# Kernel tuning notes

Measured on AMD Instinct MI355X. Metric: run time of the kernel, lower is better.

## Reference

```python
import jax, jax.numpy as jnp
import numpy as np

GROUPS = 8   # channels // group_size with group_size=8 for C=64
EPS = 1e-5


def group_norm_qc(x0, x1, gamma, beta):
    """LatticeGroupNorm: stats computed jointly over both cosets per (batch, group)."""
    B, C, H, W = x0.shape
    g = GROUPS
    xg = jnp.concatenate([x0.reshape(B, g, -1), x1.reshape(B, g, -1)], axis=-1)
    mean = xg.mean(axis=-1).reshape(B, g, 1, 1, 1)
    var = xg.var(axis=-1).reshape(B, g, 1, 1, 1)
    inv = jax.lax.rsqrt(var + EPS)
    ga = gamma[None, :, None, None]
    be = beta[None, :, None, None]

    def norm(x):
        xr = x.reshape(B, g, C // g, H, W)
        return ((xr - mean) * inv).reshape(B, C, H, W) * ga + be

    return norm(x0), norm(x1)


def qc_conv(x0, x1, w_center, w_corner, bias):
    """Quincunx LatticePad+LatticeConvolution with stencil
    [(0,0),(2,0),(0,2),(2,2),(1,1)], center (1,1).
    w_center: [O,I] tap (1,1) (same-coset 1x1).
    w_corner: [O,I,2,2] taps (0,0),(2,0),(0,2),(2,2) (cross-coset 2x2).
    Pad keeps output cosets the same size as inputs ('same' lattice conv)."""
    dn = ('NCHW', 'OIHW', 'NCHW')

    def c1(x):
        return jnp.einsum('oi,bihw->bohw', w_center, x)

    def c2(x, pad):
        return jax.lax.conv_general_dilated(x, w_corner, (1, 1), pad,
                                            dimension_numbers=dn)

    b = bias[None, :, None, None]
    # coset0 output gathers coset1 at (i-1+a, j-1+b) -> pad top/left
    out0 = c1(x0) + c2(x1, ((1, 0), (1, 0))) + b
    # coset1 output gathers coset0 at (i+a, j+b) -> pad bottom/right
    out1 = c1(x1) + c2(x0, ((0, 1), (0, 1))) + b
    return out0, out1


def setup_inputs() -> dict:
    key = jax.random.key(0)
    ks = jax.random.split(key, 10)
    B, C, H, W = 2, 64, 256, 256
    s = 0.05
    return {
        'x0': jax.random.normal(ks[0], (B, C, H, W), jnp.float32),
        'x1': jax.random.normal(ks[1], (B, C, H, W), jnp.float32),
        'g1': jnp.ones((C,), jnp.float32),
        'b1': jnp.zeros((C,), jnp.float32),
        'w1_center': jax.random.normal(ks[2], (C, C), jnp.float32) * s,
        'w1_corner': jax.random.normal(ks[3], (C, C, 2, 2), jnp.float32) * s,
        'bias1': jax.random.normal(ks[4], (C,), jnp.float32) * s,
        'g2': jnp.ones((C,), jnp.float32),
        'b2': jnp.zeros((C,), jnp.float32),
        'w2_center': jax.random.normal(ks[5], (C, C), jnp.float32) * s,
        'w2_corner': jax.random.normal(ks[6], (C, C, 2, 2), jnp.float32) * s,
        'bias2': jax.random.normal(ks[7], (C,), jnp.float32) * s,
        'w_skip': jax.random.normal(ks[8], (C, C), jnp.float32) * s,
        'bias_skip': jax.random.normal(ks[9], (C,), jnp.float32) * s,
        'g_skip': jnp.ones((C,), jnp.float32),
        'beta_skip': jnp.zeros((C,), jnp.float32),
    }


def reference(x0, x1, g1, b1, w1_center, w1_corner, bias1,
              g2, b2, w2_center, w2_corner, bias2,
              w_skip, bias_skip, g_skip, beta_skip):
    # conv path: GN -> ReLU -> pad+conv -> GN -> ReLU -> pad+conv
    h0, h1 = group_norm_qc(x0, x1, g1, b1)
    h0, h1 = jax.nn.relu(h0), jax.nn.relu(h1)
    h0, h1 = qc_conv(h0, h1, w1_center, w1_corner, bias1)
    h0, h1 = group_norm_qc(h0, h1, g2, b2)
    h0, h1 = jax.nn.relu(h0), jax.nn.relu(h1)
    h0, h1 = qc_conv(h0, h1, w2_center, w2_corner, bias2)
    # skip path: 1x1 lattice conv (stencil [(0,0)]) -> GN
    bsk = bias_skip[None, :, None, None]
    s0 = jnp.einsum('oi,bihw->bohw', w_skip, x0) + bsk
    s1 = jnp.einsum('oi,bihw->bohw', w_skip, x1) + bsk
    s0, s1 = group_norm_qc(s0, s1, g_skip, beta_skip)
    # residual add; stack the two cosets as leading axis for a single output
    return jnp.stack([h0 + s0, h1 + s1])
```

## Files before the change

### kernel.cpp

```cpp
#include <hip/hip_runtime.h>

typedef __attribute__((ext_vector_type(8))) __bf16 bf16x8;
typedef __attribute__((ext_vector_type(4))) __bf16 bf16x4;
typedef __attribute__((ext_vector_type(4))) float f32x4;

#define MFMA16(a,b,c) __builtin_amdgcn_mfma_f32_16x16x32_bf16(a,b,c,0,0,0)

static constexpr int HW = 65536;
static constexpr int WD = 256;
static constexpr int NB = 2;
static constexpr double INV_N = 1.0 / 1048576.0;
static constexpr float EPSV = 1e-5f;

static constexpr size_t OFF_P1  = 0;
static constexpr size_t OFF_P2  = 131072;
static constexpr size_t OFF_A1  = 200704;
static constexpr size_t OFF_A2  = OFF_A1 + 40960;
static constexpr size_t OFF_XT  = OFF_A2 + 40960;
static constexpr size_t SZ_T    = (size_t)2 * NB * HW * 64 * 2;
static constexpr size_t OFF_S   = OFF_XT + SZ_T;
static constexpr size_t OFF_H   = OFF_S + SZ_T;

#define TL8(base, px, c) (*(const bf16x8*)&(base)[(px) * 64 + (((c)) ^ ((((px)) & 7) << 3))])

__global__ __launch_bounds__(256, 4) void K1(
    const float* __restrict__ x0, const float* __restrict__ x1,
    const float* __restrict__ wskip, const float* __restrict__ bskip,
    const float* __restrict__ wc1, const float* __restrict__ wk1,
    const float* __restrict__ wc2, const float* __restrict__ wk2,
    __bf16* __restrict__ xt, __bf16* __restrict__ sout,
    __bf16* __restrict__ A1, __bf16* __restrict__ A2, float* __restrict__ p1) {
  const int bx = blockIdx.x;
  const int t = threadIdx.x;

  if (bx >= 1024) {
    const int stage = bx - 1024;
    const float* wc = stage ? wc2 : wc1;
    const float* wk = stage ? wk2 : wk1;
    __bf16* A = stage ? A2 : A1;
    for (int idx = t; idx < 64 * 320; idx += 256) {
      int o = idx / 320, k = idx - o * 320;
      float v;
      if (k < 64) v = wc[o * 64 + k];
      else v = wk[(o * 64 + (k & 63)) * 4 + ((k - 64) >> 6)];
      A[idx] = (__bf16)v;
    }
    return;
  }

  const int row = bx & 255, b = (bx >> 8) & 1, co = bx >> 9;
  const float* x = co ? x1 : x0;
  __shared__ __attribute__((aligned(16))) __bf16 tile[256 * 64];
  __shared__ float redp[256];
  __shared__ float reds[32];
  const int wv = t >> 6, lane = t & 63;
  const float* xbase = x + (size_t)b * 64 * HW + (size_t)row * WD + t;
  __bf16* xtbase = xt + (((size_t)(co * NB + b) * HW) + (size_t)row * WD + t) * 64;

  float gsum[8], gsq[8];
#pragma unroll
  for (int g = 0; g < 8; ++g) { gsum[g] = 0.f; gsq[g] = 0.f; }
#pragma unroll
  for (int hf = 0; hf < 2; ++hf) {
    float f[32];
#pragma unroll
    for (int k = 0; k < 32; ++k) f[k] = xbase[(size_t)(hf * 32 + k) * HW];
    __builtin_amdgcn_sched_barrier(0);
#pragma unroll
    for (int c4 = 0; c4 < 4; ++c4) {
      const int cg = hf * 4 + c4;
      bf16x8 v;
#pragma unroll
      for (int j = 0; j < 8; ++j) {
        float xv = f[c4 * 8 + j];
        v[j] = (__bf16)xv;
        gsum[cg] += xv;
        gsq[cg] = fmaf(xv, xv, gsq[cg]);
      }
      *(bf16x8*)&tile[t * 64 + ((cg ^ (t & 7)) * 8)] = v;
      *(bf16x8*)&xtbase[cg * 8] = v;
    }
  }
#pragma unroll
  for (int g = 0; g < 8; ++g) {
#pragma unroll
    for (int m = 1; m < 16; m <<= 1) {
      gsum[g] += __shfl_xor(gsum[g], m, 64);
      gsq[g]  += __shfl_xor(gsq[g], m, 64);
    }
  }
  {
    const int q0 = lane >> 4;
    if ((lane & 15) == 0) {
#pragma unroll
      for (int g = 0; g < 8; ++g) {
        redp[(wv * 4 + q0) * 16 + g] = gsum[g];
        redp[(wv * 4 + q0) * 16 + 8 + g] = gsq[g];
      }
    }
  }
  __syncthreads();

  const int ln = lane & 15, q = lane >> 4;
  bf16x8 a0, a1;
#pragma unroll
  for (int j = 0; j < 8; ++j) {
    a0[j] = (__bf16)wskip[(wv * 16 + ln) * 64 + q * 8 + j];
    a1[j] = (__bf16)wskip[(wv * 16 + ln) * 64 + 32 + q * 8 + j];
  }
  float bia[4];
#pragma unroll
  for (int r = 0; r < 4; ++r) bia[r] = bskip[wv * 16 + q * 4 + r];

  float ssum = 0.f, ssq = 0.f;
  for (int n = 0; n < 16; ++n) {
    f32x4 acc = {0.f, 0.f, 0.f, 0.f};
    const int px = n * 16 + ln;
    bf16x8 b0 = TL8(tile, px, q * 8);
    bf16x8 b1 = TL8(tile, px, q * 8 + 32);
    acc = MFMA16(a0, b0, acc);
    acc = MFMA16(a1, b1, acc);
    bf16x4 sv;
#pragma unroll
    for (int r = 0; r < 4; ++r) {
      float v = acc[r] + bia[r];
      ssum += v;
      ssq = fmaf(v, v, ssq);
      sv[r] = (__bf16)v;
    }
    size_t sb = ((size_t)(co * NB + b) * 4096 + row * 16 + n) * 1024 + (wv * 4 + q) * 64 + ln * 4;
    *(bf16x4*)&sout[sb] = sv;
  }
#pragma unroll
  for (int m = 1; m < 16; m <<= 1) {
    ssum += __shfl_xor(ssum, m, 64);
    ssq  += __shfl_xor(ssq, m, 64);
  }
  if ((lane & 15) == 0) {
    reds[wv * 4 + q] = ssum;
    reds[16 + wv * 4 + q] = ssq;
  }
  __syncthreads();
  if (t < 32) {
    float val;
    if (t < 16) {
      val = 0.f;
#pragma unroll
      for (int k = 0; k < 16; ++k) val += redp[k * 16 + t];
    } else {
      int kind = (t >> 3) & 1, g = t & 7;
      int wvv = g >> 1, qp = g & 1;
      val = reds[kind * 16 + wvv * 4 + qp * 2] + reds[kind * 16 + wvv * 4 + qp * 2 + 1];
    }
    p1[(size_t)((co * 2 + b) * 256 + row) * 32 + t] = val;
  }
}

__global__ __launch_bounds__(256, 4) void K2(
    const __bf16* __restrict__ xt, const __bf16* __restrict__ A1,
    const float* __restrict__ p1, const float* __restrict__ g1, const float* __restrict__ be1,
    const float* __restrict__ bias1,
    __bf16* __restrict__ h, float* __restrict__ p2) {
  const int blk = ((blockIdx.x & 7) << 6) | (blockIdx.x >> 3);
  const int tx = blk & 15, ty = blk >> 4;
  const int b = blockIdx.y;
  const int y0p = ty * 8, x0p = tx * 16;
  __shared__ __attribute__((aligned(16))) __bf16 tl[2][153 * 64];
  __shared__ float sc[64], sh[64];
  __shared__ float lst[16];
  __shared__ double redn[16];
  const int t = threadIdx.x;

  if (t < 16) lst[t] = 0.f;
  {
    const int col = t >> 4, sub = t & 15;
    double v = 0.0;
    for (int j = sub; j < 512; j += 16) {
      int cc = j >> 8, rr2 = j & 255;
      v += (double)p1[((size_t)(cc * 2 + b) * 256 + rr2) * 32 + col];
    }
    v += __shfl_xor(v, 1, 64);
    v += __shfl_xor(v, 2, 64);
    v += __shfl_xor(v, 4, 64);
    v += __shfl_xor(v, 8, 64);
    if (sub == 0) redn[col] = v;
  }
  __syncthreads();
  if (t < 64) {
    int g = t >> 3;
    double mean = redn[g] * INV_N;
    double var  = redn[8 + g] * INV_N - mean * mean;
    float inv = rsqrtf((float)var + EPSV);
    float s_ = inv * g1[t];
    sc[t] = s_;
    sh[t] = be1[t] - (float)mean * s_;
  }
  __syncthreads();

#pragma unroll
  for (int i = 0; i < 10; ++i) {
    int u = t + i * 256;
    if (u < 2 * 153 * 8) {
      int cs = u / 1224;
      int rr = u - cs * 1224;
      int px = rr >> 3, cg = rr & 7;
      int ly = px / 17, lx = px - ly * 17;
      int gy = y0p + ly - cs, gx = x0p + lx - cs;
      bf16x8 v;
#pragma unroll
      for (int j = 0; j < 8; ++j) v[j] = (__bf16)0.f;
      if ((unsigned)gy < 256u && (unsigned)gx < 256u) {
        bf16x8 raw = *(const bf16x8*)&xt[(((size_t)(cs * NB + b) * WD + gy) * WD + gx) * 64 + cg * 8];
#pragma unroll
        for (int j = 0; j < 8; ++j) {
          float f = fmaf((float)raw[j], sc[cg * 8 + j], sh[cg * 8 + j]);
          v[j] = (__bf16)fmaxf(f, 0.f);
        }
      }
      *(bf16x8*)&tl[cs][px * 64 + ((cg ^ (px & 7)) * 8)] = v;
    }
  }

  const int wv = t >> 6, lane = t & 63, ln = lane & 15, q = lane >> 4;
  const int co = wv & 1, mh = wv >> 1;
  const int q8 = q * 8;
  bf16x8 af[2][10];
#pragma unroll
  for (int m = 0; m < 2; ++m)
#pragma unroll
    for (int kk = 0; kk < 10; ++kk)
      af[m][kk] = *(const bf16x8*)&A1[(mh * 32 + m * 16 + ln) * 320 + kk * 32 + q8];
  __syncthreads();

  f32x4 acc[8][2];
#pragma unroll
  for (int n = 0; n < 8; ++n)
#pragma unroll
    for (int m = 0; m < 2; ++m) acc[n][m] = (f32x4){0.f, 0.f, 0.f, 0.f};

  const __bf16* tc = tl[co];
  const __bf16* to = tl[1 - co];
#pragma unroll
  for (int n = 0; n < 8; ++n) {
    const int cpix = co ? ((n + 1) * 17 + ln + 1) : (n * 17 + ln);
    const int tb = n * 17 + ln;
    bf16x8 bb;
    bb = TL8(tc, cpix, q8);          acc[n][0]=MFMA16(af[0][0],bb,acc[n][0]); acc[n][1]=MFMA16(af[1][0],bb,acc[n][1]);
    bb = TL8(tc, cpix, q8 + 32);     acc[n][0]=MFMA16(af[0][1],bb,acc[n][0]); acc[n][1]=MFMA16(af[1][1],bb,acc[n][1]);
    bb = TL8(to, tb, q8);            acc[n][0]=MFMA16(af[0][2],bb,acc[n][0]); acc[n][1]=MFMA16(af[1][2],bb,acc[n][1]);
    bb = TL8(to, tb, q8 + 32);       acc[n][0]=MFMA16(af[0][3],bb,acc[n][0]); acc[n][1]=MFMA16(af[1][3],bb,acc[n][1]);
    bb = TL8(to, tb + 1, q8);        acc[n][0]=MFMA16(af[0][4],bb,acc[n][0]); acc[n][1]=MFMA16(af[1][4],bb,acc[n][1]);
    bb = TL8(to, tb + 1, q8 + 32);   acc[n][0]=MFMA16(af[0][5],bb,acc[n][0]); acc[n][1]=MFMA16(af[1][5],bb,acc[n][1]);
    bb = TL8(to, tb + 17, q8);       acc[n][0]=MFMA16(af[0][6],bb,acc[n][0]); acc[n][1]=MFMA16(af[1][6],bb,acc[n][1]);
    bb = TL8(to, tb + 17, q8 + 32);  acc[n][0]=MFMA16(af[0][7],bb,acc[n][0]); acc[n][1]=MFMA16(af[1][7],bb,acc[n][1]);
    bb = TL8(to, tb + 18, q8);       acc[n][0]=MFMA16(af[0][8],bb,acc[n][0]); acc[n][1]=MFMA16(af[1][8],bb,acc[n][1]);
    bb = TL8(to, tb + 18, q8 + 32);  acc[n][0]=MFMA16(af[0][9],bb,acc[n][0]); acc[n][1]=MFMA16(af[1][9],bb,acc[n][1]);
  }

  __syncthreads();

  float s2s[2] = {0.f, 0.f}, s2q[2] = {0.f, 0.f};
  float bia[2][4];
#pragma unroll
  for (int m = 0; m < 2; ++m)
#pragma unroll
    for (int r = 0; r < 4; ++r) bia[m][r] = bias1[mh * 32 + m * 16 + q * 4 + r];

#pragma unroll
  for (int n = 0; n < 8; ++n)
#pragma unroll
    for (int m = 0; m < 2; ++m) {
      bf16x4 hv;
#pragma unroll
      for (int r = 0; r < 4; ++r) {
        float v = acc[n][m][r] + bia[m][r];
        s2s[m] += v;
        s2q[m] = fmaf(v, v, s2q[m]);
        hv[r] = (__bf16)v;
      }
      *(bf16x4*)&tl[co][(n * 16 + ln) * 64 + ((mh * 32 + m * 16 + q * 4) ^ ((ln & 7) << 3))] = hv;
    }

#pragma unroll
  for (int m = 0; m < 2; ++m) {
    float a_ = s2s[m], c_ = s2q[m];
#pragma unroll
    for (int mk = 1; mk < 32; mk <<= 1) {
      a_ += __shfl_xor(a_, mk, 64);
      c_ += __shfl_xor(c_, mk, 64);
    }
    if ((lane & 31) == 0) {
      int g = mh * 4 + m * 2 + (q >> 1);
      atomicAdd(&lst[g], a_);
      atomicAdd(&lst[8 + g], c_);
    }
  }
  __syncthreads();

#pragma unroll
  for (int i = 0; i < 8; ++i) {
    int co2 = i >> 2;
    int idx = (i & 3) * 256 + t;
    int px = idx >> 3, chunk = idx & 7;
    int gy = y0p + (px >> 4), gx = x0p + (px & 15);
    bf16x8 vv = *(const bf16x8*)&tl[co2][px * 64 + ((chunk ^ (px & 7)) * 8)];
    *(bf16x8*)&h[(((size_t)(co2 * NB + b) * WD + gy) * WD + gx) * 64 + chunk * 8] = vv;
  }

  if (t < 16) p2[((size_t)b * 512 + blockIdx.x) * 16 + t] = lst[t];
}

__global__ __launch_bounds__(256, 4) void K3(
    const __bf16* __restrict__ hin, const __bf16* __restrict__ A2,
    const float* __restrict__ p2, const float* __restrict__ p1,
    const float* __restrict__ g2, const float* __restrict__ be2, const float* __restrict__ bias2,
    const float* __restrict__ gsk, const float* __restrict__ besk,
    const __bf16* __restrict__ sin_, float* __restrict__ out) {
  const int blk = ((blockIdx.x & 7) << 6) | (blockIdx.x >> 3);
  const int tx = blk & 15, ty = blk >> 4;
  const int b = blockIdx.y;
  const int y0p = ty * 8, x0p = tx * 16;
  __shared__ __attribute__((aligned(16))) __bf16 tl[2][153 * 64];
  __shared__ float sc2[64], sh2[64], scS[64], shS[64];
  __shared__ double redn[32];
  const int t = threadIdx.x;

  {
    const int col = t >> 3, sub = t & 7;
    double v = 0.0;
    if (col < 16) {
      for (int j = sub; j < 512; j += 8)
        v += (double)p2[((size_t)b * 512 + j) * 16 + col];
    } else {
      for (int j = sub; j < 512; j += 8) {
        int cc = j >> 8, rr2 = j & 255;
        v += (double)p1[((size_t)(cc * 2 + b) * 256 + rr2) * 32 + col];
      }
    }
    v += __shfl_xor(v, 1, 64);
    v += __shfl_xor(v, 2, 64);
    v += __shfl_xor(v, 4, 64);
    if (sub == 0) redn[col] = v;
  }
  __syncthreads();
  if (t < 128) {
    int half = t >> 6, ch = t & 63, g = ch >> 3;
    if (half == 0) {
      double mean = redn[g] * INV_N;
      double var  = redn[8 + g] * INV_N - mean * mean;
      float inv = rsqrtf((float)var + EPSV);
      float s_ = inv * g2[ch];
      sc2[ch] = s_;
      sh2[ch] = be2[ch] - (float)mean * s_;
    } else {
      double mean = redn[16 + g] * INV_N;
      double var  = redn[24 + g] * INV_N - mean * mean;
      float inv = rsqrtf((float)var + EPSV);
      float s_ = inv * gsk[ch];
      scS[ch] = s_;
      shS[ch] = besk[ch] - (float)mean * s_;
    }
  }
  __syncthreads();

#pragma unroll
  for (int i = 0; i < 10; ++i) {
    int u = t + i * 256;
    if (u < 2 * 153 * 8) {
      int cs = u / 1224;
      int rr = u - cs * 1224;
      int px = rr >> 3, cg = rr & 7;
      int ly = px / 17, lx = px - ly * 17;
      int gy = y0p + ly - cs, gx = x0p + lx - cs;
      bf16x8 v;
#pragma unroll
      for (int j = 0; j < 8; ++j) v[j] = (__bf16)0.f;
      if ((unsigned)gy < 256u && (unsigned)gx < 256u) {
        bf16x8 raw = *(const bf16x8*)&hin[(((size_t)(cs * NB + b) * WD + gy) * WD + gx) * 64 + cg * 8];
#pragma unroll
        for (int j = 0; j < 8; ++j) {
          float f = fmaf((float)raw[j], sc2[cg * 8 + j], sh2[cg * 8 + j]);
          v[j] = (__bf16)fmaxf(f, 0.f);
        }
      }
      *(bf16x8*)&tl[cs][px * 64 + ((cg ^ (px & 7)) * 8)] = v;
    }
  }

  const int wv = t >> 6, lane = t & 63, ln = lane & 15, q = lane >> 4;
  const int co = wv & 1, mh = wv >> 1;
  const int q8 = q * 8;
  bf16x8 af[2][10];
#pragma unroll
  for (int m = 0; m < 2; ++m)
#pragma unroll
    for (int kk = 0; kk < 10; ++kk)
      af[m][kk] = *(const bf16x8*)&A2[(mh * 32 + m * 16 + ln) * 320 + kk * 32 + q8];
  __syncthreads();

  f32x4 acc[8][2];
#pragma unroll
  for (int n = 0; n < 8; ++n)
#pragma unroll
    for (int m = 0; m < 2; ++m) acc[n][m] = (f32x4){0.f, 0.f, 0.f, 0.f};

  const __bf16* tc = tl[co];
  const __bf16* to = tl[1 - co];
#pragma unroll
  for (int n = 0; n < 8; ++n) {
    const int cpix = co ? ((n + 1) * 17 + ln + 1) : (n * 17 + ln);
    const int tb = n * 17 + ln;
    bf16x8 bb;
    bb = TL8(tc, cpix, q8);          acc[n][0]=MFMA16(af[0][0],bb,acc[n][0]); acc[n][1]=MFMA16(af[1][0],bb,acc[n][1]);
    bb = TL8(tc, cpix, q8 + 32);     acc[n][0]=MFMA16(af[0][1],bb,acc[n][0]); acc[n][1]=MFMA16(af[1][1],bb,acc[n][1]);
    bb = TL8(to, tb, q8);            acc[n][0]=MFMA16(af[0][2],bb,acc[n][0]); acc[n][1]=MFMA16(af[1][2],bb,acc[n][1]);
    bb = TL8(to, tb, q8 + 32);       acc[n][0]=MFMA16(af[0][3],bb,acc[n][0]); acc[n][1]=MFMA16(af[1][3],bb,acc[n][1]);
    bb = TL8(to, tb + 1, q8);        acc[n][0]=MFMA16(af[0][4],bb,acc[n][0]); acc[n][1]=MFMA16(af[1][4],bb,acc[n][1]);
    bb = TL8(to, tb + 1, q8 + 32);   acc[n][0]=MFMA16(af[0][5],bb,acc[n][0]); acc[n][1]=MFMA16(af[1][5],bb,acc[n][1]);
    bb = TL8(to, tb + 17, q8);       acc[n][0]=MFMA16(af[0][6],bb,acc[n][0]); acc[n][1]=MFMA16(af[1][6],bb,acc[n][1]);
    bb = TL8(to, tb + 17, q8 + 32);  acc[n][0]=MFMA16(af[0][7],bb,acc[n][0]); acc[n][1]=MFMA16(af[1][7],bb,acc[n][1]);
    bb = TL8(to, tb + 18, q8);       acc[n][0]=MFMA16(af[0][8],bb,acc[n][0]); acc[n][1]=MFMA16(af[1][8],bb,acc[n][1]);
    bb = TL8(to, tb + 18, q8 + 32);  acc[n][0]=MFMA16(af[0][9],bb,acc[n][0]); acc[n][1]=MFMA16(af[1][9],bb,acc[n][1]);
  }

  float bia[2][4], sA[2][4], sB[2][4];
#pragma unroll
  for (int m = 0; m < 2; ++m)
#pragma unroll
    for (int r = 0; r < 4; ++r) {
      int ch = mh * 32 + m * 16 + q * 4 + r;
      bia[m][r] = bias2[ch];
      sA[m][r] = scS[ch];
      sB[m][r] = shS[ch];
    }

#pragma unroll
  for (int n = 0; n < 8; ++n) {
    int gy = y0p + n;
#pragma unroll
    for (int m = 0; m < 2; ++m) {
      int ch0 = mh * 32 + m * 16 + q * 4;
      size_t sb = ((size_t)(co * NB + b) * 4096 + gy * 16 + tx) * 1024 + (mh * 8 + m * 4 + q) * 64 + ln * 4;
      bf16x4 sv = *(const bf16x4*)&sin_[sb];
      size_t ob = ((size_t)(co * NB + b) * 64 + ch0) * HW + (size_t)gy * WD + x0p + ln;
#pragma unroll
      for (int r = 0; r < 4; ++r) {
        float v = acc[n][m][r] + bia[m][r] + fmaf((float)sv[r], sA[m][r], sB[m][r]);
        out[ob + (size_t)r * HW] = v;
      }
    }
  }
}

extern "C" void kernel_launch(void* const* d_in, const int* in_sizes, int n_in,
                              void* d_out, int out_size, void* d_ws, size_t ws_size,
                              hipStream_t stream) {
  (void)in_sizes; (void)n_in; (void)out_size; (void)ws_size;
  const float* x0    = (const float*)d_in[0];
  const float* x1    = (const float*)d_in[1];
  const float* g1    = (const float*)d_in[2];
  const float* b1    = (const float*)d_in[3];
  const float* w1c   = (const float*)d_in[4];
  const float* w1k   = (const float*)d_in[5];
  const float* bias1 = (const float*)d_in[6];
  const float* g2    = (const float*)d_in[7];
  const float* b2    = (const float*)d_in[8];
  const float* w2c   = (const float*)d_in[9];
  const float* w2k   = (const float*)d_in[10];
  const float* bias2 = (const float*)d_in[11];
  const float* wsk   = (const float*)d_in[12];
  const float* bsk   = (const float*)d_in[13];
  const float* gsk   = (const float*)d_in[14];
  const float* besk  = (const float*)d_in[15];

  char* ws = (char*)d_ws;
  float*  p1 = (float*)(ws + OFF_P1);
  float*  p2 = (float*)(ws + OFF_P2);
  __bf16* A1 = (__bf16*)(ws + OFF_A1);
  __bf16* A2 = (__bf16*)(ws + OFF_A2);
  __bf16* xt = (__bf16*)(ws + OFF_XT);
  __bf16* s  = (__bf16*)(ws + OFF_S);
  __bf16* h  = (__bf16*)(ws + OFF_H);

  K1<<<dim3(1026), 256, 0, stream>>>(x0, x1, wsk, bsk, w1c, w1k, w2c, w2k, xt, s, A1, A2, p1);
  K2<<<dim3(512, 2), 256, 0, stream>>>(xt, A1, p1, g1, b1, bias1, h, p2);
  K3<<<dim3(512, 2), 256, 0, stream>>>(h, A2, p2, p1, g2, b2, bias2, gsk, besk, s, (float*)d_out);
}
```

Baseline: 324.1 us.

## Recompute skip conv in K3 from transposed input instead of storing skip output

```diff
diff --git a/kernel.cpp b/kernel.cpp
--- a/kernel.cpp
+++ b/kernel.cpp
@@ -16,10 +16,10 @@
 static constexpr size_t OFF_P2  = 131072;
 static constexpr size_t OFF_A1  = 200704;
 static constexpr size_t OFF_A2  = OFF_A1 + 40960;
-static constexpr size_t OFF_XT  = OFF_A2 + 40960;
+static constexpr size_t OFF_AS  = OFF_A2 + 40960;
+static constexpr size_t OFF_XT  = OFF_AS + 8192;
 static constexpr size_t SZ_T    = (size_t)2 * NB * HW * 64 * 2;
-static constexpr size_t OFF_S   = OFF_XT + SZ_T;
-static constexpr size_t OFF_H   = OFF_S + SZ_T;
+static constexpr size_t OFF_H   = OFF_XT + SZ_T;
 
 #define TL8(base, px, c) (*(const bf16x8*)&(base)[(px) * 64 + (((c)) ^ ((((px)) & 7) << 3))])
 
@@ -28,22 +28,35 @@
     const float* __restrict__ wskip, const float* __restrict__ bskip,
     const float* __restrict__ wc1, const float* __restrict__ wk1,
     const float* __restrict__ wc2, const float* __restrict__ wk2,
-    __bf16* __restrict__ xt, __bf16* __restrict__ sout,
-    __bf16* __restrict__ A1, __bf16* __restrict__ A2, float* __restrict__ p1) {
+    __bf16* __restrict__ xt,
+    __bf16* __restrict__ A1, __bf16* __restrict__ A2, __bf16* __restrict__ Ask,
+    float* __restrict__ p1) {
   const int bx = blockIdx.x;
   const int t = threadIdx.x;
 
   if (bx >= 1024) {
     const int stage = bx - 1024;
-    const float* wc = stage ? wc2 : wc1;
-    const float* wk = stage ? wk2 : wk1;
-    __bf16* A = stage ? A2 : A1;
-    for (int idx = t; idx < 64 * 320; idx += 256) {
-      int o = idx / 320, k = idx - o * 320;
-      float v;
-      if (k < 64) v = wc[o * 64 + k];
-      else v = wk[(o * 64 + (k & 63)) * 4 + ((k - 64) >> 6)];
-      A[idx] = (__bf16)v;
+    if (stage == 0) {
+      for (int idx = t; idx < 64 * 320 + 64 * 64; idx += 256) {
+        if (idx < 64 * 320) {
+          int o = idx / 320, k = idx - o * 320;
+          float v;
+          if (k < 64) v = wc1[o * 64 + k];
+          else v = wk1[(o * 64 + (k & 63)) * 4 + ((k - 64) >> 6)];
+          A1[idx] = (__bf16)v;
+        } else {
+          int e = idx - 64 * 320;
+          Ask[e] = (__bf16)wskip[e];
+        }
+      }
+    } else {
+      for (int idx = t; idx < 64 * 320; idx += 256) {
+        int o = idx / 320, k = idx - o * 320;
+        float v;
+        if (k < 64) v = wc2[o * 64 + k];
+        else v = wk2[(o * 64 + (k & 63)) * 4 + ((k - 64) >> 6)];
+        A2[idx] = (__bf16)v;
+      }
     }
     return;
   }
@@ -120,16 +133,12 @@
     bf16x8 b1 = TL8(tile, px, q * 8 + 32);
     acc = MFMA16(a0, b0, acc);
     acc = MFMA16(a1, b1, acc);
-    bf16x4 sv;
 #pragma unroll
     for (int r = 0; r < 4; ++r) {
       float v = acc[r] + bia[r];
       ssum += v;
       ssq = fmaf(v, v, ssq);
-      sv[r] = (__bf16)v;
-    }
-    size_t sb = ((size_t)(co * NB + b) * 4096 + row * 16 + n) * 1024 + (wv * 4 + q) * 64 + ln * 4;
-    *(bf16x4*)&sout[sb] = sv;
+    }
   }
 #pragma unroll
   for (int m = 1; m < 16; m <<= 1) {
@@ -312,10 +321,11 @@
 
 __global__ __launch_bounds__(256, 4) void K3(
     const __bf16* __restrict__ hin, const __bf16* __restrict__ A2,
+    const __bf16* __restrict__ xt, const __bf16* __restrict__ Ask,
     const float* __restrict__ p2, const float* __restrict__ p1,
     const float* __restrict__ g2, const float* __restrict__ be2, const float* __restrict__ bias2,
-    const float* __restrict__ gsk, const float* __restrict__ besk,
-    const __bf16* __restrict__ sin_, float* __restrict__ out) {
+    const float* __restrict__ gsk, const float* __restrict__ besk, const float* __restrict__ bskip,
+    float* __restrict__ out) {
   const int blk = ((blockIdx.x & 7) << 6) | (blockIdx.x >> 3);
   const int tx = blk & 15, ty = blk >> 4;
   const int b = blockIdx.y;
@@ -423,7 +433,14 @@
     bb = TL8(to, tb + 18, q8 + 32);  acc[n][0]=MFMA16(af[0][9],bb,acc[n][0]); acc[n][1]=MFMA16(af[1][9],bb,acc[n][1]);
   }
 
-  float bia[2][4], sA[2][4], sB[2][4];
+  bf16x8 aS[2][2];
+#pragma unroll
+  for (int m = 0; m < 2; ++m)
+#pragma unroll
+    for (int hh = 0; hh < 2; ++hh)
+      aS[m][hh] = *(const bf16x8*)&Ask[(mh * 32 + m * 16 + ln) * 64 + hh * 32 + q8];
+
+  float bia[2][4], sA[2][4], sBp[2][4];
 #pragma unroll
   for (int m = 0; m < 2; ++m)
 #pragma unroll
@@ -431,22 +448,36 @@
       int ch = mh * 32 + m * 16 + q * 4 + r;
       bia[m][r] = bias2[ch];
       sA[m][r] = scS[ch];
-      sB[m][r] = shS[ch];
-    }
-
-#pragma unroll
-  for (int n = 0; n < 8; ++n) {
-    int gy = y0p + n;
-#pragma unroll
-    for (int m = 0; m < 2; ++m) {
-      int ch0 = mh * 32 + m * 16 + q * 4;
-      size_t sb = ((size_t)(co * NB + b) * 4096 + gy * 16 + tx) * 1024 + (mh * 8 + m * 4 + q) * 64 + ln * 4;
-      bf16x4 sv = *(const bf16x4*)&sin_[sb];
-      size_t ob = ((size_t)(co * NB + b) * 64 + ch0) * HW + (size_t)gy * WD + x0p + ln;
-#pragma unroll
-      for (int r = 0; r < 4; ++r) {
-        float v = acc[n][m][r] + bia[m][r] + fmaf((float)sv[r], sA[m][r], sB[m][r]);
-        out[ob + (size_t)r * HW] = v;
+      sBp[m][r] = fmaf(scS[ch], bskip[ch], shS[ch]);
+    }
+
+#pragma unroll
+  for (int ng = 0; ng < 2; ++ng) {
+    bf16x8 xb[4][2];
+#pragma unroll
+    for (int nn = 0; nn < 4; ++nn) {
+      int gy = y0p + ng * 4 + nn;
+#pragma unroll
+      for (int hh = 0; hh < 2; ++hh)
+        xb[nn][hh] = *(const bf16x8*)&xt[(((size_t)(co * NB + b) * WD + gy) * WD + x0p + ln) * 64 + hh * 32 + q8];
+    }
+    __builtin_amdgcn_sched_barrier(0);
+#pragma unroll
+    for (int nn = 0; nn < 4; ++nn) {
+      int n = ng * 4 + nn;
+      int gy = y0p + n;
+#pragma unroll
+      for (int m = 0; m < 2; ++m) {
+        f32x4 accS = {0.f, 0.f, 0.f, 0.f};
+        accS = MFMA16(aS[m][0], xb[nn][0], accS);
+        accS = MFMA16(aS[m][1], xb[nn][1], accS);
+        int ch0 = mh * 32 + m * 16 + q * 4;
+        size_t ob = ((size_t)(co * NB + b) * 64 + ch0) * HW + (size_t)gy * WD + x0p + ln;
+#pragma unroll
+        for (int r = 0; r < 4; ++r) {
+          float v = acc[n][m][r] + bia[m][r] + fmaf(accS[r], sA[m][r], sBp[m][r]);
+          out[ob + (size_t)r * HW] = v;
+        }
       }
     }
   }
@@ -478,11 +509,11 @@
   float*  p2 = (float*)(ws + OFF_P2);
   __bf16* A1 = (__bf16*)(ws + OFF_A1);
   __bf16* A2 = (__bf16*)(ws + OFF_A2);
+  __bf16* As = (__bf16*)(ws + OFF_AS);
   __bf16* xt = (__bf16*)(ws + OFF_XT);
-  __bf16* s  = (__bf16*)(ws + OFF_S);
   __bf16* h  = (__bf16*)(ws + OFF_H);
 
-  K1<<<dim3(1026), 256, 0, stream>>>(x0, x1, wsk, bsk, w1c, w1k, w2c, w2k, xt, s, A1, A2, p1);
+  K1<<<dim3(1026), 256, 0, stream>>>(x0, x1, wsk, bsk, w1c, w1k, w2c, w2k, xt, A1, A2, As, p1);
   K2<<<dim3(512, 2), 256, 0, stream>>>(xt, A1, p1, g1, b1, bias1, h, p2);
-  K3<<<dim3(512, 2), 256, 0, stream>>>(h, A2, p2, p1, g2, b2, bias2, gsk, besk, s, (float*)d_out);
+  K3<<<dim3(512, 2), 256, 0, stream>>>(h, A2, xt, As, p2, p1, g2, b2, bias2, gsk, besk, bsk, (float*)d_out);
 }
```

Result: no change. 326.4 us (+0.7%).
